# Optimization experiments

Hardware: AMD Instinct MI355X
Metric: run time of the kernel (lower is better)

Reference implementation:

```python
import jax, jax.numpy as jnp
import numpy as np

EMBED = 2048
HEADS = 16
DHEAD = EMBED // HEADS


def setup_inputs() -> dict:
    key = jax.random.key(0)
    k1, k2, k3 = jax.random.split(key, 3)
    x = jax.random.normal(k1, (4, 2048, EMBED), dtype=jnp.float32)
    # torch Linear weight layout: [out_features, in_features]; y = x @ W.T
    W_in = jax.random.normal(k2, (3 * EMBED, EMBED), dtype=jnp.float32) * (EMBED ** -0.5)
    W_out = jax.random.normal(k3, (EMBED, EMBED), dtype=jnp.float32) * (EMBED ** -0.5)
    return {"x": x, "W_in": W_in, "W_out": W_out}


def reference(x, W_in, W_out):
    B, T, C = x.shape
    qkv = jnp.einsum('btc,fc->btf', x, W_in)          # [B,T,3C]
    q, k, v = jnp.split(qkv, 3, axis=-1)
    def heads(t):
        return t.reshape(B, T, HEADS, DHEAD).transpose(0, 2, 1, 3)  # [B,H,T,D]
    q, k, v = heads(q), heads(k), heads(v)
    scale = DHEAD ** -0.5
    scores = jnp.einsum('bhtd,bhsd->bhts', q, k) * scale  # [B,H,T,T]
    causal = jnp.tril(jnp.ones((T, T), dtype=bool))
    scores = jnp.where(causal, scores, jnp.finfo(scores.dtype).min)
    attn = jax.nn.softmax(scores, axis=-1)
    y = jnp.einsum('bhts,bhsd->bhtd', attn, v)            # [B,H,T,D]
    y = y.transpose(0, 2, 1, 3).reshape(B, T, C)
    return jnp.einsum('btc,fc->btf', y, W_out)
```

## Files before the change

### kernel.cpp

```cpp
#include <hip/hip_runtime.h>

typedef unsigned short u16;
typedef unsigned int u32;
typedef __attribute__((ext_vector_type(8))) short bf16x8;
typedef __attribute__((ext_vector_type(4))) float f32x4;
typedef __attribute__((ext_vector_type(8))) unsigned short u16x8;
typedef __attribute__((ext_vector_type(4))) u32 u32x4;

#define MFMA16 __builtin_amdgcn_mfma_f32_16x16x32_bf16

__device__ __forceinline__ u16 f2bf(float f) {
  unsigned u = __float_as_uint(f);
  u += 0x7fffu + ((u >> 16) & 1u);
  return (u16)(u >> 16);
}

__device__ __forceinline__ void async16(void* lds, const void* g) {
  __builtin_amdgcn_global_load_lds(
      (const __attribute__((address_space(1))) unsigned int*)g,
      (__attribute__((address_space(3))) unsigned int*)lds, 16, 0, 0);
}

__global__ void convert_bf16(const float* __restrict__ in, u16* __restrict__ out, int n4) {
  int i = blockIdx.x * blockDim.x + threadIdx.x;
  int st = gridDim.x * blockDim.x;
  for (; i < n4; i += st) {
    float4 f = ((const float4*)in)[i];
    ushort4 o;
    o.x = f2bf(f.x); o.y = f2bf(f.y); o.z = f2bf(f.z); o.w = f2bf(f.w);
    ((ushort4*)out)[i] = o;
  }
}

#define GEMM256_CORE(A_, B_)                                                    \
  __shared__ __align__(16) char lds[131072];                                    \
  const int tid = threadIdx.x;                                                  \
  const int lane = tid & 63, w = tid >> 6;                                      \
  const int wr = w >> 2, wc = w & 3;                                            \
  const int fr = lane & 15, fq = lane >> 4;                                     \
  const int lrA = tid >> 3, ccA = tid & 7, w8 = w << 3;                         \
  f32x4 acc[8][4] = {};                                                         \
  const u16* Abase = A_ + (size_t)tm * 2048;                                    \
  const u16* Bbase = B_ + (size_t)tn * 2048;                                    \
  auto stageA = [&](int mh, int kt, char* buf) {                                \
    _Pragma("unroll") for (int it = 0; it < 2; ++it) {                          \
      int lrt = it * 64 + lrA;                                                  \
      int row = mh * 64 + (lrt & 63) + ((lrt & 64) << 1);                       \
      const u16* src = Abase + (size_t)row * 2048 + kt + ((ccA ^ (row & 7)) << 3); \
      int lr0 = it * 64 + w8;                                                   \
      int row0 = mh * 64 + (lr0 & 63) + ((lr0 & 64) << 1);                      \
      async16(buf + row0 * 128, src);                                           \
    }                                                                           \
  };                                                                            \
  auto stageB = [&](int nh, int kt, char* buf) {                                \
    _Pragma("unroll") for (int it = 0; it < 2; ++it) {                          \
      int lrt = it * 64 + lrA;                                                  \
      int nr = ((lrt >> 5) << 6) + nh * 32 + (lrt & 31);                        \
      const u16* src = Bbase + (size_t)nr * 2048 + kt + ((ccA ^ (nr & 7)) << 3); \
      int lr0 = it * 64 + w8;                                                   \
      int nr0 = ((lr0 >> 5) << 6) + nh * 32 + (lr0 & 31);                       \
      async16(buf + 32768 + nr0 * 128, src);                                    \
    }                                                                           \
  };                                                                            \
  stageA(0, 0, lds); stageB(0, 0, lds); stageB(1, 0, lds); stageA(1, 0, lds);   \
  for (int t = 0; t < 32; ++t) {                                                \
    char* cur = lds + (t & 1) * 65536;                                          \
    char* nxt = lds + ((t + 1) & 1) * 65536;                                    \
    const int ktn = (t + 1) * 64;                                               \
    const bool more = (t + 1 < 32);                                             \
    _Pragma("unroll") for (int p = 0; p < 4; ++p) {                             \
      const int mh = p >> 1, nh = (p == 1 || p == 2) ? 1 : 0;                   \
      if (p < 3) asm volatile("s_waitcnt vmcnt(4)" ::: "memory");               \
      __builtin_amdgcn_s_barrier();                                             \
      asm volatile("" ::: "memory");                                            \
      bf16x8 af[4][2], bfr[2][2];                                               \
      _Pragma("unroll") for (int i = 0; i < 4; ++i) {                           \
        int rr = wr * 128 + mh * 64 + i * 16 + fr;                              \
        _Pragma("unroll") for (int ks = 0; ks < 2; ++ks)                        \
          af[i][ks] = *(const bf16x8*)(cur + rr * 128 +                         \
                                       (((ks * 4 + fq) ^ (rr & 7)) << 4));      \
      }                                                                         \
      _Pragma("unroll") for (int j = 0; j < 2; ++j) {                           \
        int nr = wc * 64 + nh * 32 + j * 16 + fr;                               \
        _Pragma("unroll") for (int ks = 0; ks < 2; ++ks)                        \
          bfr[j][ks] = *(const bf16x8*)(cur + 32768 + nr * 128 +                \
                                        (((ks * 4 + fq) ^ (nr & 7)) << 4));     \
      }                                                                         \
      if (more) {                                                               \
        if (p == 0) stageA(0, ktn, nxt);                                        \
        else if (p == 1) stageB(0, ktn, nxt);                                   \
        else if (p == 2) stageB(1, ktn, nxt);                                   \
        else stageA(1, ktn, nxt);                                               \
      }                                                                         \
      __builtin_amdgcn_s_setprio(1);                                            \
      _Pragma("unroll") for (int ks = 0; ks < 2; ++ks)                          \
        _Pragma("unroll") for (int i = 0; i < 4; ++i)                           \
          _Pragma("unroll") for (int j = 0; j < 2; ++j)                         \
            acc[mh * 4 + i][nh * 2 + j] = MFMA16(af[i][ks], bfr[j][ks],         \
                                                 acc[mh * 4 + i][nh * 2 + j],   \
                                                 0, 0, 0);                      \
      __builtin_amdgcn_s_setprio(0);                                            \
    }                                                                           \
  }

__global__ __launch_bounds__(512, 2) void gemm_qkv8(
    const u16* __restrict__ A, const u16* __restrict__ B,
    u16* __restrict__ Qb, u16* __restrict__ Kb, u16* __restrict__ Vb) {
  int id = blockIdx.x;
  int swz = (id & 7) * 96 + (id >> 3);
  const int tm = (swz / 24) * 256, tn = (swz % 24) * 256;
  GEMM256_CORE(A, B)
#pragma unroll
  for (int J = 0; J < 4; ++J) {
    int n = tn + wc * 64 + J * 16 + fr;
    int which = n >> 11, h = (n >> 7) & 15, d = n & 127;
    u16* dst = which == 0 ? Qb : (which == 1 ? Kb : Vb);
#pragma unroll
    for (int I = 0; I < 8; ++I)
#pragma unroll
      for (int rr = 0; rr < 4; ++rr) {
        int m = tm + wr * 128 + I * 16 + fq * 4 + rr;
        int bb = m >> 11, tt = m & 2047;
        dst[((size_t)((bb * 16 + h) * 2048 + tt) << 7) + d] = f2bf(acc[I][J][rr]);
      }
  }
}

__global__ __launch_bounds__(512, 2) void gemm_out8(
    const u16* __restrict__ A, const u16* __restrict__ B, float* __restrict__ C) {
  int id = blockIdx.x;
  int swz = (id & 7) * 32 + (id >> 3);
  const int tm = (swz / 8) * 256, tn = (swz % 8) * 256;
  GEMM256_CORE(A, B)
#pragma unroll
  for (int J = 0; J < 4; ++J) {
    int n = tn + wc * 64 + J * 16 + fr;
#pragma unroll
    for (int I = 0; I < 8; ++I)
#pragma unroll
      for (int rr = 0; rr < 4; ++rr) {
        int m = tm + wr * 128 + I * 16 + fq * 4 + rr;
        C[(size_t)m * 2048 + n] = acc[I][J][rr];
      }
  }
}

__global__ __launch_bounds__(256) void transpose_v(const u16* __restrict__ V,
                                                   u16* __restrict__ Vt) {
  __shared__ u16 lds[64 * 72];
  const int tid = threadIdx.x;
  const int pair = blockIdx.z;
  const int t0 = blockIdx.x * 64, d0 = blockIdx.y * 64;
  const u16* Vp = V + (size_t)pair * 262144;
  u16* Vtp = Vt + (size_t)pair * 262144;
#pragma unroll
  for (int it = 0; it < 2; ++it) {
    int c = it * 256 + tid;
    int t = c >> 3, ch = c & 7;
    u16x8 tv = *(const u16x8*)&Vp[(size_t)(t0 + t) * 128 + d0 + ch * 8];
#pragma unroll
    for (int jj = 0; jj < 8; ++jj) lds[(ch * 8 + jj) * 72 + t] = tv[jj];
  }
  __syncthreads();
#pragma unroll
  for (int it = 0; it < 2; ++it) {
    int c = it * 256 + tid;
    int d = c >> 3, ct = c & 7;
    u16x8 tv = *(const u16x8*)&lds[d * 72 + ct * 8];
    *(u16x8*)&Vtp[(size_t)(d0 + d) * 2048 + t0 + ct * 8] = tv;
  }
}

__global__ __launch_bounds__(512, 4) void attn8(
    const u16* __restrict__ Q, const u16* __restrict__ K,
    const u16* __restrict__ Vt, u16* __restrict__ Y) {
  __shared__ __align__(16) char smem[49152];
  char* lK = smem;
  char* lV = smem + 16384;
  char* lP = smem + 32768;
  const int tid = threadIdx.x;
  const int lane = tid & 63, w = tid >> 6;
  const int fr = lane & 15, fq = lane >> 4;
  const int pair = blockIdx.x, by = blockIdx.y;
  const size_t hoff = (size_t)pair * 262144;
  const u16* Qh = Q + hoff;
  const u16* Kh = K + hoff;
  const u16* Vth = Vt + hoff;
  const int b = pair >> 4, h = pair & 15;
  const float c1 = 0.08838834764831845f * 1.4426950408889634f;
  const float THR = 11.5f;

  int ksr[2], kcc[2], vdr[2], vcc[2];
#pragma unroll
  for (int it = 0; it < 2; ++it) {
    int idx = it * 512 + tid;
    ksr[it] = idx >> 4; kcc[it] = idx & 15;
    vdr[it] = idx >> 3; vcc[it] = idx & 7;
  }

  for (int phase = 0; phase < 2; ++phase) {
    const int qb = phase ? 15 - by : by;
    const int q0 = qb * 128;
    const int nt = 2 * qb + 2;
    const int qw = q0 + w * 16;

    bf16x8 qf[4];
#pragma unroll
    for (int ks = 0; ks < 4; ++ks)
      qf[ks] = *(const bf16x8*)&Qh[(size_t)(qw + fr) * 128 + ks * 32 + fq * 8];

    f32x4 o[8] = {};
    float m2[4], ls[4];
#pragma unroll
    for (int r = 0; r < 4; ++r) { m2[r] = -1e30f; ls[r] = 0.f; }

    u32x4 kst[2], vst[2];
#pragma unroll
    for (int it = 0; it < 2; ++it) {
      kst[it] = *(const u32x4*)&Kh[(size_t)ksr[it] * 128 + kcc[it] * 8];
      vst[it] = *(const u32x4*)&Vth[(size_t)vdr[it] * 2048 + vcc[it] * 8];
    }

    for (int t = 0; t < nt; ++t) {
      const int kv0 = t * 64;
#pragma unroll
      for (int it = 0; it < 2; ++it) {
        *(u32x4*)(lK + ksr[it] * 256 + ((kcc[it] ^ (ksr[it] & 7)) << 4)) = kst[it];
        *(u32x4*)(lV + vdr[it] * 128 + ((vcc[it] ^ (vdr[it] & 7)) << 4)) = vst[it];
      }
      if (t + 1 < nt) {
        const int nk = kv0 + 64;
#pragma unroll
        for (int it = 0; it < 2; ++it) {
          kst[it] = *(const u32x4*)&Kh[(size_t)(nk + ksr[it]) * 128 + kcc[it] * 8];
          vst[it] = *(const u32x4*)&Vth[(size_t)vdr[it] * 2048 + nk + vcc[it] * 8];
        }
      }
      __syncthreads();

      if (kv0 <= qw + 15) {
        f32x4 sc[4] = {};
#pragma unroll
        for (int j = 0; j < 4; ++j) {
          int s = j * 16 + fr;
#pragma unroll
          for (int ks = 0; ks < 4; ++ks) {
            bf16x8 kf = *(const bf16x8*)(lK + s * 256 + (((ks * 32 + fq * 8) * 2) ^ ((s & 7) << 4)));
            sc[j] = MFMA16(qf[ks], kf, sc[j], 0, 0, 0);
          }
        }
        if (kv0 + 64 > qw) {
          int rowb = qw + fq * 4;
#pragma unroll
          for (int j = 0; j < 4; ++j) {
            int col = kv0 + j * 16 + fr;
#pragma unroll
            for (int r = 0; r < 4; ++r)
              if (col > rowb + r) sc[j][r] = -3e38f;
          }
        }
        float lmax[4];
        bool trip = false;
#pragma unroll
        for (int r = 0; r < 4; ++r) {
          lmax[r] = fmaxf(fmaxf(sc[0][r], sc[1][r]), fmaxf(sc[2][r], sc[3][r]));
          trip = trip || (lmax[r] * c1 > m2[r] + THR);
        }
        if (__any(trip)) {
#pragma unroll
          for (int r = 0; r < 4; ++r) {
            float v = lmax[r];
            v = fmaxf(v, __shfl_xor(v, 1));
            v = fmaxf(v, __shfl_xor(v, 2));
            v = fmaxf(v, __shfl_xor(v, 4));
            v = fmaxf(v, __shfl_xor(v, 8));
            v *= c1;
            float mn = fmaxf(m2[r], v);
            float corr = __builtin_amdgcn_exp2f(m2[r] - mn);
            m2[r] = mn;
            ls[r] *= corr;
#pragma unroll
            for (int n = 0; n < 8; ++n) o[n][r] *= corr;
          }
        }
#pragma unroll
        for (int r = 0; r < 4; ++r) {
          int prow = w * 16 + fq * 4 + r;
          float rs = 0.f;
#pragma unroll
          for (int j = 0; j < 4; ++j) {
            float p = __builtin_amdgcn_exp2f(sc[j][r] * c1 - m2[r]);
            rs += p;
            *(u16*)(lP + prow * 128 + (((j * 16 + fr) * 2) ^ ((prow & 7) << 4))) = f2bf(p);
          }
          ls[r] += rs;
        }
        bf16x8 pf[2];
        {
          int prow = w * 16 + fr;
#pragma unroll
          for (int k2 = 0; k2 < 2; ++k2)
            pf[k2] = *(const bf16x8*)(lP + prow * 128 + ((k2 * 64 + fq * 16) ^ ((prow & 7) << 4)));
        }
#pragma unroll
        for (int n = 0; n < 8; ++n) {
          int d = n * 16 + fr;
#pragma unroll
          for (int k2 = 0; k2 < 2; ++k2) {
            bf16x8 vf = *(const bf16x8*)(lV + d * 128 + ((k2 * 64 + fq * 16) ^ ((d & 7) << 4)));
            o[n] = MFMA16(pf[k2], vf, o[n], 0, 0, 0);
          }
        }
      }
      __syncthreads();
    }

    float inv[4];
#pragma unroll
    for (int r = 0; r < 4; ++r) {
      float s = ls[r];
      s += __shfl_xor(s, 1);
      s += __shfl_xor(s, 2);
      s += __shfl_xor(s, 4);
      s += __shfl_xor(s, 8);
      inv[r] = 1.f / s;
    }
#pragma unroll
    for (int n = 0; n < 8; ++n)
#pragma unroll
      for (int r = 0; r < 4; ++r) {
        int tt = qw + fq * 4 + r;
        Y[((size_t)(b * 2048 + tt) * 2048) + h * 128 + n * 16 + fr] = f2bf(o[n][r] * inv[r]);
      }
  }
}

extern "C" void kernel_launch(void* const* d_in, const int* in_sizes, int n_in,
                              void* d_out, int out_size, void* d_ws, size_t ws_size,
                              hipStream_t stream) {
  const float* x = (const float*)d_in[0];
  const float* Win = (const float*)d_in[1];
  const float* Wout = (const float*)d_in[2];
  float* out = (float*)d_out;
  char* ws = (char*)d_ws;

  u16* x_bf   = (u16*)(ws);
  u16* win_bf = (u16*)(ws + 33554432);
  u16* wout_bf= (u16*)(ws + 58720256);
  u16* Qb     = (u16*)(ws + 67108864);
  u16* Kb     = (u16*)(ws + 100663296);
  u16* Vb     = (u16*)(ws + 134217728);
  u16* y_bf   = (u16*)(ws + 167772160);
  u16* Vtb    = x_bf;

  convert_bf16<<<2048, 256, 0, stream>>>(x, x_bf, 16777216 / 4);
  convert_bf16<<<2048, 256, 0, stream>>>(Win, win_bf, 12582912 / 4);
  convert_bf16<<<1024, 256, 0, stream>>>(Wout, wout_bf, 4194304 / 4);

  gemm_qkv8<<<768, 512, 0, stream>>>(x_bf, win_bf, Qb, Kb, Vb);
  transpose_v<<<dim3(32, 2, 64), 256, 0, stream>>>(Vb, Vtb);
  attn8<<<dim3(64, 8), 512, 0, stream>>>(Qb, Kb, Vtb, y_bf);
  gemm_out8<<<256, 512, 0, stream>>>(y_bf, wout_bf, out);
}
```

Baseline: 541.0 us.

## Read V fragments directly from global memory and drop paired-phase attention blocks

The attention kernel no longer stages V tiles in LDS. Each wave loads its V-transpose fragments straight from global memory (with a one-step register prefetch across the d-chunks), which cuts LDS use from 48KB to 32KB. The old scheme, where each block handled two query blocks (qb and 15-qb) to balance causal work, is replaced by one query block per block on a 64x16 grid, with the heaviest blocks launched first. This trades LDS traffic and pressure for redundant global/L2 reads of V by every wave, and it loses the explicit load balancing from pairing.

```diff
diff --git a/kernel.cpp b/kernel.cpp
--- a/kernel.cpp
+++ b/kernel.cpp
@@ -171,17 +171,17 @@
   }
 }
 
-__global__ __launch_bounds__(512, 4) void attn8(
+__global__ __launch_bounds__(512, 4) void attn9(
     const u16* __restrict__ Q, const u16* __restrict__ K,
     const u16* __restrict__ Vt, u16* __restrict__ Y) {
-  __shared__ __align__(16) char smem[49152];
+  __shared__ __align__(16) char smem[32768];
   char* lK = smem;
-  char* lV = smem + 16384;
-  char* lP = smem + 32768;
+  char* lP = smem + 16384;
   const int tid = threadIdx.x;
   const int lane = tid & 63, w = tid >> 6;
   const int fr = lane & 15, fq = lane >> 4;
-  const int pair = blockIdx.x, by = blockIdx.y;
+  const int pair = blockIdx.x;
+  const int qb = 15 - blockIdx.y;
   const size_t hoff = (size_t)pair * 262144;
   const u16* Qh = Q + hoff;
   const u16* Kh = K + hoff;
@@ -190,149 +190,144 @@
   const float c1 = 0.08838834764831845f * 1.4426950408889634f;
   const float THR = 11.5f;
 
-  int ksr[2], kcc[2], vdr[2], vcc[2];
+  int ksr[2], kcc[2];
 #pragma unroll
   for (int it = 0; it < 2; ++it) {
     int idx = it * 512 + tid;
     ksr[it] = idx >> 4; kcc[it] = idx & 15;
-    vdr[it] = idx >> 3; vcc[it] = idx & 7;
-  }
-
-  for (int phase = 0; phase < 2; ++phase) {
-    const int qb = phase ? 15 - by : by;
-    const int q0 = qb * 128;
-    const int nt = 2 * qb + 2;
-    const int qw = q0 + w * 16;
-
-    bf16x8 qf[4];
-#pragma unroll
-    for (int ks = 0; ks < 4; ++ks)
-      qf[ks] = *(const bf16x8*)&Qh[(size_t)(qw + fr) * 128 + ks * 32 + fq * 8];
-
-    f32x4 o[8] = {};
-    float m2[4], ls[4];
-#pragma unroll
-    for (int r = 0; r < 4; ++r) { m2[r] = -1e30f; ls[r] = 0.f; }
-
-    u32x4 kst[2], vst[2];
-#pragma unroll
-    for (int it = 0; it < 2; ++it) {
-      kst[it] = *(const u32x4*)&Kh[(size_t)ksr[it] * 128 + kcc[it] * 8];
-      vst[it] = *(const u32x4*)&Vth[(size_t)vdr[it] * 2048 + vcc[it] * 8];
+  }
+
+  const int q0 = qb * 128;
+  const int nt = 2 * qb + 2;
+  const int qw = q0 + w * 16;
+
+  bf16x8 qf[4];
+#pragma unroll
+  for (int ks = 0; ks < 4; ++ks)
+    qf[ks] = *(const bf16x8*)&Qh[(size_t)(qw + fr) * 128 + ks * 32 + fq * 8];
+
+  f32x4 o[8] = {};
+  float m2[4], ls[4];
+#pragma unroll
+  for (int r = 0; r < 4; ++r) { m2[r] = -1e30f; ls[r] = 0.f; }
+
+  u32x4 kst[2];
+#pragma unroll
+  for (int it = 0; it < 2; ++it)
+    kst[it] = *(const u32x4*)&Kh[(size_t)ksr[it] * 128 + kcc[it] * 8];
+
+  for (int t = 0; t < nt; ++t) {
+    const int kv0 = t * 64;
+#pragma unroll
+    for (int it = 0; it < 2; ++it)
+      *(u32x4*)(lK + ksr[it] * 256 + ((kcc[it] ^ (ksr[it] & 7)) << 4)) = kst[it];
+    if (t + 1 < nt) {
+      const int nk = kv0 + 64;
+#pragma unroll
+      for (int it = 0; it < 2; ++it)
+        kst[it] = *(const u32x4*)&Kh[(size_t)(nk + ksr[it]) * 128 + kcc[it] * 8];
     }
-
-    for (int t = 0; t < nt; ++t) {
-      const int kv0 = t * 64;
-#pragma unroll
-      for (int it = 0; it < 2; ++it) {
-        *(u32x4*)(lK + ksr[it] * 256 + ((kcc[it] ^ (ksr[it] & 7)) << 4)) = kst[it];
-        *(u32x4*)(lV + vdr[it] * 128 + ((vcc[it] ^ (vdr[it] & 7)) << 4)) = vst[it];
-      }
-      if (t + 1 < nt) {
-        const int nk = kv0 + 64;
-#pragma unroll
-        for (int it = 0; it < 2; ++it) {
-          kst[it] = *(const u32x4*)&Kh[(size_t)(nk + ksr[it]) * 128 + kcc[it] * 8];
-          vst[it] = *(const u32x4*)&Vth[(size_t)vdr[it] * 2048 + nk + vcc[it] * 8];
-        }
-      }
-      __syncthreads();
-
-      if (kv0 <= qw + 15) {
-        f32x4 sc[4] = {};
+    __syncthreads();
+
+    if (kv0 <= qw + 15) {
+      f32x4 sc[4] = {};
+#pragma unroll
+      for (int j = 0; j < 4; ++j) {
+        int s = j * 16 + fr;
+#pragma unroll
+        for (int ks = 0; ks < 4; ++ks) {
+          bf16x8 kf = *(const bf16x8*)(lK + s * 256 + (((ks * 32 + fq * 8) * 2) ^ ((s & 7) << 4)));
+          sc[j] = MFMA16(qf[ks], kf, sc[j], 0, 0, 0);
+        }
+      }
+      if (kv0 + 64 > qw) {
+        int rowb = qw + fq * 4;
 #pragma unroll
         for (int j = 0; j < 4; ++j) {
-          int s = j * 16 + fr;
-#pragma unroll
-          for (int ks = 0; ks < 4; ++ks) {
-            bf16x8 kf = *(const bf16x8*)(lK + s * 256 + (((ks * 32 + fq * 8) * 2) ^ ((s & 7) << 4)));
-            sc[j] = MFMA16(qf[ks], kf, sc[j], 0, 0, 0);
-          }
-        }
-        if (kv0 + 64 > qw) {
-          int rowb = qw + fq * 4;
-#pragma unroll
-          for (int j = 0; j < 4; ++j) {
-            int col = kv0 + j * 16 + fr;
-#pragma unroll
-            for (int r = 0; r < 4; ++r)
-              if (col > rowb + r) sc[j][r] = -3e38f;
-          }
-        }
-        float lmax[4];
-        bool trip = false;
+          int col = kv0 + j * 16 + fr;
+#pragma unroll
+          for (int r = 0; r < 4; ++r)
+            if (col > rowb + r) sc[j][r] = -3e38f;
+        }
+      }
+      float lmax[4];
+      bool trip = false;
+#pragma unroll
+      for (int r = 0; r < 4; ++r) {
+        lmax[r] = fmaxf(fmaxf(sc[0][r], sc[1][r]), fmaxf(sc[2][r], sc[3][r]));
+        trip = trip || (lmax[r] * c1 > m2[r] + THR);
+      }
+      if (__any(trip)) {
 #pragma unroll
         for (int r = 0; r < 4; ++r) {
-          lmax[r] = fmaxf(fmaxf(sc[0][r], sc[1][r]), fmaxf(sc[2][r], sc[3][r]));
-          trip = trip || (lmax[r] * c1 > m2[r] + THR);
-        }
-        if (__any(trip)) {
-#pragma unroll
-          for (int r = 0; r < 4; ++r) {
-            float v = lmax[r];
-            v = fmaxf(v, __shfl_xor(v, 1));
-            v = fmaxf(v, __shfl_xor(v, 2));
-            v = fmaxf(v, __shfl_xor(v, 4));
-            v = fmaxf(v, __shfl_xor(v, 8));
-            v *= c1;
-            float mn = fmaxf(m2[r], v);
-            float corr = __builtin_amdgcn_exp2f(m2[r] - mn);
-            m2[r] = mn;
-            ls[r] *= corr;
-#pragma unroll
-            for (int n = 0; n < 8; ++n) o[n][r] *= corr;
-          }
-        }
-#pragma unroll
-        for (int r = 0; r < 4; ++r) {
-          int prow = w * 16 + fq * 4 + r;
-          float rs = 0.f;
-#pragma unroll
-          for (int j = 0; j < 4; ++j) {
-            float p = __builtin_amdgcn_exp2f(sc[j][r] * c1 - m2[r]);
-            rs += p;
-            *(u16*)(lP + prow * 128 + (((j * 16 + fr) * 2) ^ ((prow & 7) << 4))) = f2bf(p);
-          }
-          ls[r] += rs;
-        }
-        bf16x8 pf[2];
-        {
-          int prow = w * 16 + fr;
-#pragma unroll
-          for (int k2 = 0; k2 < 2; ++k2)
-            pf[k2] = *(const bf16x8*)(lP + prow * 128 + ((k2 * 64 + fq * 16) ^ ((prow & 7) << 4)));
-        }
-#pragma unroll
-        for (int n = 0; n < 8; ++n) {
-          int d = n * 16 + fr;
-#pragma unroll
-          for (int k2 = 0; k2 < 2; ++k2) {
-            bf16x8 vf = *(const bf16x8*)(lV + d * 128 + ((k2 * 64 + fq * 16) ^ ((d & 7) << 4)));
-            o[n] = MFMA16(pf[k2], vf, o[n], 0, 0, 0);
-          }
-        }
-      }
-      __syncthreads();
+          float v = lmax[r];
+          v = fmaxf(v, __shfl_xor(v, 1));
+          v = fmaxf(v, __shfl_xor(v, 2));
+          v = fmaxf(v, __shfl_xor(v, 4));
+          v = fmaxf(v, __shfl_xor(v, 8));
+          v *= c1;
+          float mn = fmaxf(m2[r], v);
+          float corr = __builtin_amdgcn_exp2f(m2[r] - mn);
+          m2[r] = mn;
+          ls[r] *= corr;
+#pragma unroll
+          for (int n = 0; n < 8; ++n) o[n][r] *= corr;
+        }
+      }
+#pragma unroll
+      for (int r = 0; r < 4; ++r) {
+        int prow = w * 16 + fq * 4 + r;
+        float rs = 0.f;
+#pragma unroll
+        for (int j = 0; j < 4; ++j) {
+          float p = __builtin_amdgcn_exp2f(sc[j][r] * c1 - m2[r]);
+          rs += p;
+          *(u16*)(lP + prow * 128 + (((j * 16 + fr) * 2) ^ ((prow & 7) << 4))) = f2bf(p);
+        }
+        ls[r] += rs;
+      }
+      bf16x8 pf[2];
+      {
+        int prow = w * 16 + fr;
+#pragma unroll
+        for (int k2 = 0; k2 < 2; ++k2)
+          pf[k2] = *(const bf16x8*)(lP + prow * 128 + ((k2 * 64 + fq * 16) ^ ((prow & 7) << 4)));
+      }
+      const u16* Vrow = Vth + kv0 + fq * 8;
+      bf16x8 va0, va1, vb0, vb1;
+      va0 = *(const bf16x8*)&Vrow[(size_t)(0 * 16 + fr) * 2048];
+      va1 = *(const bf16x8*)&Vrow[(size_t)(0 * 16 + fr) * 2048 + 32];
+#pragma unroll
+      for (int n = 0; n < 8; ++n) {
+        if (n < 7) {
+          vb0 = *(const bf16x8*)&Vrow[(size_t)((n + 1) * 16 + fr) * 2048];
+          vb1 = *(const bf16x8*)&Vrow[(size_t)((n + 1) * 16 + fr) * 2048 + 32];
+        }
+        o[n] = MFMA16(pf[0], va0, o[n], 0, 0, 0);
+        o[n] = MFMA16(pf[1], va1, o[n], 0, 0, 0);
+        va0 = vb0; va1 = vb1;
+      }
     }
-
-    float inv[4];
+    __syncthreads();
+  }
+
+  float inv[4];
+#pragma unroll
+  for (int r = 0; r < 4; ++r) {
+    float s = ls[r];
+    s += __shfl_xor(s, 1);
+    s += __shfl_xor(s, 2);
+    s += __shfl_xor(s, 4);
+    s += __shfl_xor(s, 8);
+    inv[r] = 1.f / s;
+  }
+#pragma unroll
+  for (int n = 0; n < 8; ++n)
 #pragma unroll
     for (int r = 0; r < 4; ++r) {
-      float s = ls[r];
-      s += __shfl_xor(s, 1);
-      s += __shfl_xor(s, 2);
-      s += __shfl_xor(s, 4);
-      s += __shfl_xor(s, 8);
-      inv[r] = 1.f / s;
+      int tt = qw + fq * 4 + r;
+      Y[((size_t)(b * 2048 + tt) * 2048) + h * 128 + n * 16 + fr] = f2bf(o[n][r] * inv[r]);
     }
-#pragma unroll
-    for (int n = 0; n < 8; ++n)
-#pragma unroll
-      for (int r = 0; r < 4; ++r) {
-        int tt = qw + fq * 4 + r;
-        Y[((size_t)(b * 2048 + tt) * 2048) + h * 128 + n * 16 + fr] = f2bf(o[n][r] * inv[r]);
-      }
-  }
 }
 
 extern "C" void kernel_launch(void* const* d_in, const int* in_sizes, int n_in,
@@ -359,6 +354,6 @@
 
   gemm_qkv8<<<768, 512, 0, stream>>>(x_bf, win_bf, Qb, Kb, Vb);
   transpose_v<<<dim3(32, 2, 64), 256, 0, stream>>>(Vb, Vtb);
-  attn8<<<dim3(64, 8), 512, 0, stream>>>(Qb, Kb, Vtb, y_bf);
+  attn9<<<dim3(64, 16), 512, 0, stream>>>(Qb, Kb, Vtb, y_bf);
   gemm_out8<<<256, 512, 0, stream>>>(y_bf, wout_bf, out);
 }
```

Measured after the change: 579.1 us. 7.1% more time.

## Fuse V transpose into QKV GEMM epilogue and halve GEMM barrier phases

Applied to the files above, without the earlier changes.

The QKV GEMM epilogue now writes V directly in transposed [d, t] layout as packed 4-element stores, which removes the separate transpose_v kernel and its extra read and write of V. The GEMM core loop also moves from four barrier phases per K-tile to two. Each phase loads all four B fragments once and reuses them across both M halves, so there are fewer barriers and fewer LDS reads. The cost is more live fragment registers, coarser overlap between staging and MFMA, and scattered 8-byte strides in the V epilogue.

```diff
diff --git a/kernel.cpp b/kernel.cpp
--- a/kernel.cpp
+++ b/kernel.cpp
@@ -5,6 +5,7 @@
 typedef __attribute__((ext_vector_type(8))) short bf16x8;
 typedef __attribute__((ext_vector_type(4))) float f32x4;
 typedef __attribute__((ext_vector_type(8))) unsigned short u16x8;
+typedef __attribute__((ext_vector_type(4))) unsigned short u16x4;
 typedef __attribute__((ext_vector_type(4))) u32 u32x4;
 
 #define MFMA16 __builtin_amdgcn_mfma_f32_16x16x32_bf16
@@ -68,44 +69,54 @@
     char* nxt = lds + ((t + 1) & 1) * 65536;                                    \
     const int ktn = (t + 1) * 64;                                               \
     const bool more = (t + 1 < 32);                                             \
-    _Pragma("unroll") for (int p = 0; p < 4; ++p) {                             \
-      const int mh = p >> 1, nh = (p == 1 || p == 2) ? 1 : 0;                   \
-      if (p < 3) asm volatile("s_waitcnt vmcnt(4)" ::: "memory");               \
-      __builtin_amdgcn_s_barrier();                                             \
-      asm volatile("" ::: "memory");                                            \
-      bf16x8 af[4][2], bfr[2][2];                                               \
-      _Pragma("unroll") for (int i = 0; i < 4; ++i) {                           \
-        int rr = wr * 128 + mh * 64 + i * 16 + fr;                              \
-        _Pragma("unroll") for (int ks = 0; ks < 2; ++ks)                        \
-          af[i][ks] = *(const bf16x8*)(cur + rr * 128 +                         \
-                                       (((ks * 4 + fq) ^ (rr & 7)) << 4));      \
-      }                                                                         \
-      _Pragma("unroll") for (int j = 0; j < 2; ++j) {                           \
-        int nr = wc * 64 + nh * 32 + j * 16 + fr;                               \
-        _Pragma("unroll") for (int ks = 0; ks < 2; ++ks)                        \
-          bfr[j][ks] = *(const bf16x8*)(cur + 32768 + nr * 128 +                \
-                                        (((ks * 4 + fq) ^ (nr & 7)) << 4));     \
-      }                                                                         \
-      if (more) {                                                               \
-        if (p == 0) stageA(0, ktn, nxt);                                        \
-        else if (p == 1) stageB(0, ktn, nxt);                                   \
-        else if (p == 2) stageB(1, ktn, nxt);                                   \
-        else stageA(1, ktn, nxt);                                               \
-      }                                                                         \
-      __builtin_amdgcn_s_setprio(1);                                            \
+                                                        \
+    asm volatile("s_waitcnt vmcnt(2)" ::: "memory");                            \
+    __builtin_amdgcn_s_barrier();                                               \
+    asm volatile("" ::: "memory");                                              \
+    bf16x8 af[4][2], bfr[4][2];                                                 \
+    _Pragma("unroll") for (int i = 0; i < 4; ++i) {                             \
+      int rr = wr * 128 + i * 16 + fr;                                          \
       _Pragma("unroll") for (int ks = 0; ks < 2; ++ks)                          \
-        _Pragma("unroll") for (int i = 0; i < 4; ++i)                           \
-          _Pragma("unroll") for (int j = 0; j < 2; ++j)                         \
-            acc[mh * 4 + i][nh * 2 + j] = MFMA16(af[i][ks], bfr[j][ks],         \
-                                                 acc[mh * 4 + i][nh * 2 + j],   \
-                                                 0, 0, 0);                      \
-      __builtin_amdgcn_s_setprio(0);                                            \
-    }                                                                           \
+        af[i][ks] = *(const bf16x8*)(cur + rr * 128 +                           \
+                                     (((ks * 4 + fq) ^ (rr & 7)) << 4));        \
+    }                                                                           \
+    _Pragma("unroll") for (int j = 0; j < 4; ++j) {                             \
+      int nr = wc * 64 + j * 16 + fr;                                           \
+      _Pragma("unroll") for (int ks = 0; ks < 2; ++ks)                          \
+        bfr[j][ks] = *(const bf16x8*)(cur + 32768 + nr * 128 +                  \
+                                      (((ks * 4 + fq) ^ (nr & 7)) << 4));       \
+    }                                                                           \
+    if (more) { stageA(0, ktn, nxt); stageB(0, ktn, nxt); }                     \
+    __builtin_amdgcn_s_setprio(1);                                              \
+    _Pragma("unroll") for (int ks = 0; ks < 2; ++ks)                            \
+      _Pragma("unroll") for (int i = 0; i < 4; ++i)                             \
+        _Pragma("unroll") for (int j = 0; j < 4; ++j)                           \
+          acc[i][j] = MFMA16(af[i][ks], bfr[j][ks], acc[i][j], 0, 0, 0);        \
+    __builtin_amdgcn_s_setprio(0);                                              \
+                                                        \
+    if (more) asm volatile("s_waitcnt vmcnt(4)" ::: "memory");                  \
+    else      asm volatile("s_waitcnt vmcnt(0)" ::: "memory");                  \
+    __builtin_amdgcn_s_barrier();                                               \
+    asm volatile("" ::: "memory");                                              \
+    bf16x8 ag[4][2];                                                            \
+    _Pragma("unroll") for (int i = 0; i < 4; ++i) {                             \
+      int rr = wr * 128 + 64 + i * 16 + fr;                                     \
+      _Pragma("unroll") for (int ks = 0; ks < 2; ++ks)                          \
+        ag[i][ks] = *(const bf16x8*)(cur + rr * 128 +                           \
+                                     (((ks * 4 + fq) ^ (rr & 7)) << 4));        \
+    }                                                                           \
+    if (more) { stageB(1, ktn, nxt); stageA(1, ktn, nxt); }                     \
+    __builtin_amdgcn_s_setprio(1);                                              \
+    _Pragma("unroll") for (int ks = 0; ks < 2; ++ks)                            \
+      _Pragma("unroll") for (int i = 0; i < 4; ++i)                             \
+        _Pragma("unroll") for (int j = 0; j < 4; ++j)                           \
+          acc[4 + i][j] = MFMA16(ag[i][ks], bfr[j][ks], acc[4 + i][j], 0, 0, 0);\
+    __builtin_amdgcn_s_setprio(0);                                              \
   }
 
 __global__ __launch_bounds__(512, 2) void gemm_qkv8(
     const u16* __restrict__ A, const u16* __restrict__ B,
-    u16* __restrict__ Qb, u16* __restrict__ Kb, u16* __restrict__ Vb) {
+    u16* __restrict__ Qb, u16* __restrict__ Kb, u16* __restrict__ Vtb) {
   int id = blockIdx.x;
   int swz = (id & 7) * 96 + (id >> 3);
   const int tm = (swz / 24) * 256, tn = (swz % 24) * 256;
@@ -114,15 +125,27 @@
   for (int J = 0; J < 4; ++J) {
     int n = tn + wc * 64 + J * 16 + fr;
     int which = n >> 11, h = (n >> 7) & 15, d = n & 127;
-    u16* dst = which == 0 ? Qb : (which == 1 ? Kb : Vb);
-#pragma unroll
-    for (int I = 0; I < 8; ++I)
-#pragma unroll
-      for (int rr = 0; rr < 4; ++rr) {
-        int m = tm + wr * 128 + I * 16 + fq * 4 + rr;
-        int bb = m >> 11, tt = m & 2047;
-        dst[((size_t)((bb * 16 + h) * 2048 + tt) << 7) + d] = f2bf(acc[I][J][rr]);
-      }
+    if (which < 2) {
+      u16* dst = which == 0 ? Qb : Kb;
+#pragma unroll
+      for (int I = 0; I < 8; ++I)
+#pragma unroll
+        for (int rr = 0; rr < 4; ++rr) {
+          int m = tm + wr * 128 + I * 16 + fq * 4 + rr;
+          int bb = m >> 11, tt = m & 2047;
+          dst[((size_t)((bb * 16 + h) * 2048 + tt) << 7) + d] = f2bf(acc[I][J][rr]);
+        }
+    } else {
+#pragma unroll
+      for (int I = 0; I < 8; ++I) {
+        int m0 = tm + wr * 128 + I * 16 + fq * 4;
+        int bb = m0 >> 11, tt0 = m0 & 2047;
+        u16x4 pk;
+#pragma unroll
+        for (int rr = 0; rr < 4; ++rr) pk[rr] = f2bf(acc[I][J][rr]);
+        *(u16x4*)&Vtb[(size_t)(bb * 16 + h) * 262144 + (size_t)d * 2048 + tt0] = pk;
+      }
+    }
   }
 }
 
@@ -142,32 +165,6 @@
         int m = tm + wr * 128 + I * 16 + fq * 4 + rr;
         C[(size_t)m * 2048 + n] = acc[I][J][rr];
       }
-  }
-}
-
-__global__ __launch_bounds__(256) void transpose_v(const u16* __restrict__ V,
-                                                   u16* __restrict__ Vt) {
-  __shared__ u16 lds[64 * 72];
-  const int tid = threadIdx.x;
-  const int pair = blockIdx.z;
-  const int t0 = blockIdx.x * 64, d0 = blockIdx.y * 64;
-  const u16* Vp = V + (size_t)pair * 262144;
-  u16* Vtp = Vt + (size_t)pair * 262144;
-#pragma unroll
-  for (int it = 0; it < 2; ++it) {
-    int c = it * 256 + tid;
-    int t = c >> 3, ch = c & 7;
-    u16x8 tv = *(const u16x8*)&Vp[(size_t)(t0 + t) * 128 + d0 + ch * 8];
-#pragma unroll
-    for (int jj = 0; jj < 8; ++jj) lds[(ch * 8 + jj) * 72 + t] = tv[jj];
-  }
-  __syncthreads();
-#pragma unroll
-  for (int it = 0; it < 2; ++it) {
-    int c = it * 256 + tid;
-    int d = c >> 3, ct = c & 7;
-    u16x8 tv = *(const u16x8*)&lds[d * 72 + ct * 8];
-    *(u16x8*)&Vtp[(size_t)(d0 + d) * 2048 + t0 + ct * 8] = tv;
   }
 }
 
@@ -349,16 +346,14 @@
   u16* wout_bf= (u16*)(ws + 58720256);
   u16* Qb     = (u16*)(ws + 67108864);
   u16* Kb     = (u16*)(ws + 100663296);
-  u16* Vb     = (u16*)(ws + 134217728);
+  u16* Vtb    = (u16*)(ws + 134217728);
   u16* y_bf   = (u16*)(ws + 167772160);
-  u16* Vtb    = x_bf;
 
   convert_bf16<<<2048, 256, 0, stream>>>(x, x_bf, 16777216 / 4);
   convert_bf16<<<2048, 256, 0, stream>>>(Win, win_bf, 12582912 / 4);
   convert_bf16<<<1024, 256, 0, stream>>>(Wout, wout_bf, 4194304 / 4);
 
-  gemm_qkv8<<<768, 512, 0, stream>>>(x_bf, win_bf, Qb, Kb, Vb);
-  transpose_v<<<dim3(32, 2, 64), 256, 0, stream>>>(Vb, Vtb);
+  gemm_qkv8<<<768, 512, 0, stream>>>(x_bf, win_bf, Qb, Kb, Vtb);
   attn8<<<dim3(64, 8), 512, 0, stream>>>(Qb, Kb, Vtb, y_bf);
   gemm_out8<<<256, 512, 0, stream>>>(y_bf, wout_bf, out);
 }
```

Result: faster. 504.3 us (-6.8%).
